# Performance work log

Hardware: AMD Instinct MI355X
Metric: run time of the kernel (lower is better)

Reference implementation:

```python
import jax, jax.numpy as jnp
import numpy as np

# fp4 e2m1 positive value grid and midpoints between adjacent grid values
_GRID = jnp.array([0.0, 0.5, 1.0, 1.5, 2.0, 3.0, 4.0, 6.0], dtype=jnp.float32)
_MIDS = jnp.array([0.25, 0.75, 1.25, 1.75, 2.5, 3.5, 5.0], dtype=jnp.float32)
BLOCK = 32               # MX block size
E8M0_BIAS = 127
F32_MIN_NORMAL = float(2.0 ** -126)
F4_E2M1_MAX_POW2 = 2     # log2 of largest power-of-two <= 6.0 -> 4.0


def _quantize_fp4(a):
    """Round-to-nearest-even onto the signed e2m1 grid."""
    mag = jnp.clip(jnp.abs(a), 0.0, 6.0)
    idx = jnp.searchsorted(_MIDS, mag, side='left')  # ties round down
    mids_pad = jnp.concatenate([_MIDS, jnp.array([-1.0], jnp.float32)])
    tie = mag == mids_pad[idx]
    idx = jnp.where(tie & (idx % 2 == 1), idx + 1, idx)  # ties-to-even mantissa
    return _GRID[idx] * jnp.where(a < 0, -1.0, 1.0)


def _floor_log2(m):
    """Exact floor(log2(m)) for m > 0, with corrections for fp rounding of log2."""
    e = jnp.floor(jnp.log2(m))
    e = jnp.where(jnp.exp2(e) > m, e - 1.0, e)
    e = jnp.where(jnp.exp2(e + 1.0) <= m, e + 1.0, e)
    return e


def _qdq_mxfp4(x):
    """Quantize-dequantize x to MX fp4_e2m1, block 32, FLOOR scale mode (to_mx + to_dtype)."""
    shp = x.shape
    xb = x.reshape(-1, BLOCK)
    max_abs = jnp.max(jnp.abs(xb), axis=1)
    eps = F32_MIN_NORMAL * (max_abs == 0).astype(jnp.float32)
    pow2 = _floor_log2(max_abs + eps)
    e_unb = jnp.clip(pow2 - F4_E2M1_MAX_POW2, -float(E8M0_BIAS), float(E8M0_BIAS) + 1.0)
    scale = jnp.maximum(jnp.exp2(e_unb), F32_MIN_NORMAL)  # [nblk]
    q = _quantize_fp4(xb / scale[:, None])
    return (q * scale[:, None]).reshape(shp)


def _dequant_weight(weight_packed, weight_scale, out_f, in_f):
    """Unpack uint8-packed fp4 (low nibble first), apply e8m0 block scales."""
    p = weight_packed.astype(jnp.int32)
    low = p & 0xF
    high = (p >> 4) & 0xF
    nib = jnp.stack([low, high], axis=-1).reshape(out_f, in_f)  # interleave low,high
    vals = _GRID[nib & 7] * jnp.where((nib & 8) > 0, -1.0, 1.0)
    s = jnp.exp2(weight_scale.astype(jnp.float32) - E8M0_BIAS)  # get_fp_scale(e8m0)
    return (vals.reshape(-1, BLOCK) * s[:, None]).reshape(out_f, in_f)


def setup_inputs() -> dict:
    key = jax.random.key(0)
    k1, k2, k3 = jax.random.split(key, 3)
    M, IN, OUT = 4096, 4096, 4096
    x = jax.random.normal(k1, (M, IN), dtype=jnp.float32)
    weight_packed = jax.random.randint(k2, (OUT, IN // 2), 0, 256, dtype=jnp.int32)
    weight_scale = jax.random.randint(k3, (OUT * IN // BLOCK,), 0, 135, dtype=jnp.int32)
    return {"x": x, "weight_packed": weight_packed, "weight_scale": weight_scale}


def reference(x, weight_packed, weight_scale):
    out_f = weight_packed.shape[0]
    in_f = weight_packed.shape[1] * 2
    xq = _qdq_mxfp4(x)                                       # qdq_mxfp4(x)
    w_dq = _dequant_weight(weight_packed, weight_scale, out_f, in_f)
    return xq @ w_dq.T                                       # matmul(x, w_dq.t())
```

## Files before the change

### kernel.cpp

```cpp
#include <hip/hip_runtime.h>
#include <stdint.h>

typedef __attribute__((ext_vector_type(4)))  int   intx4;
typedef __attribute__((ext_vector_type(8)))  int   intx8;
typedef __attribute__((ext_vector_type(16))) float floatx16;

#define GLL16(gp, lp)                                                               \
    __builtin_amdgcn_global_load_lds((const __attribute__((address_space(1))) unsigned int*)(gp), \
                                     (__attribute__((address_space(3))) unsigned int*)(lp), 16, 0, 0)
#define GLL4(gp, lp)                                                                \
    __builtin_amdgcn_global_load_lds((const __attribute__((address_space(1))) unsigned int*)(gp), \
                                     (__attribute__((address_space(3))) unsigned int*)(lp), 4, 0, 0)

__device__ __forceinline__ uint32_t enc1(float xv, float inv) {
    float a = fminf(fabsf(xv) * inv, 6.0f);
    int e;
    if (a < 2.0f)      e = (int)rintf(a + a);
    else if (a < 4.0f) e = (int)rintf(a) + 2;
    else               e = (int)rintf(a * 0.5f) + 4;
    return (uint32_t)e | ((__float_as_uint(xv) >> 28) & 8u);
}

__global__ __launch_bounds__(256) void prep_kernel(const float* __restrict__ x,
                                                   uint32_t* __restrict__ xq,
                                                   uint8_t* __restrict__ xs_t,
                                                   int nq, int M,
                                                   const int* __restrict__ wp,
                                                   uint32_t* __restrict__ wrep,
                                                   int nwb,
                                                   const int* __restrict__ wsc,
                                                   uint8_t* __restrict__ ws_t,
                                                   int N, int Ck) {
    const int bid = blockIdx.x;
    const int t = threadIdx.x;
    if (bid < nq) {
        const int gl = bid * 256 + t;
        const float4 v = ((const float4*)x)[gl];
        float m = fmaxf(fmaxf(fabsf(v.x), fabsf(v.y)), fmaxf(fabsf(v.z), fabsf(v.w)));
        m = fmaxf(m, __shfl_xor(m, 1));
        m = fmaxf(m, __shfl_xor(m, 2));
        m = fmaxf(m, __shfl_xor(m, 4));
        const unsigned ef = __float_as_uint(m) >> 23;
        const unsigned code = (ef < 3u) ? 1u : (ef - 2u);
        const float inv = __uint_as_float((254u - code) << 23);
        const uint32_t p = enc1(v.x, inv)        | (enc1(v.y, inv) << 4)
                         | (enc1(v.z, inv) << 8) | (enc1(v.w, inv) << 12);
        ((uint16_t*)xq)[gl] = (uint16_t)p;
        if ((gl & 7) == 0) {
            const int blk = gl >> 3;
            xs_t[(size_t)(blk & 127) * M + (blk >> 7)] = (uint8_t)code;
        }
        return;
    }
    if (bid < nq + nwb) {
        const int i = (bid - nq) * 256 + t;
        const int4 p = ((const int4*)wp)[i];
        wrep[i] = (uint32_t)(p.x & 0xFF) | ((uint32_t)(p.y & 0xFF) << 8)
                | ((uint32_t)(p.z & 0xFF) << 16) | ((uint32_t)(p.w & 0xFF) << 24);
        return;
    }
    __shared__ uint8_t raw[128 * 32];
    const int tidx = bid - nq - nwb;
    const int n0 = (tidx & 31) * 128;
    const int c0 = (tidx >> 5) * 32;
    {
        const int r = t >> 1, hf = t & 1;
        const size_t base = (size_t)(n0 + r) * Ck + c0 + hf * 16;
        uint32_t b[4];
#pragma unroll
        for (int j = 0; j < 4; ++j) {
            const int4 p = *(const int4*)(wsc + base + 4 * j);
            b[j] = (uint32_t)(p.x & 0xFF) | ((uint32_t)(p.y & 0xFF) << 8)
                 | ((uint32_t)(p.z & 0xFF) << 16) | ((uint32_t)(p.w & 0xFF) << 24);
        }
        *(uint4*)(raw + r * 32 + hf * 16) = make_uint4(b[0], b[1], b[2], b[3]);
    }
    __syncthreads();
    const int c = t >> 3, q = t & 7;
    uint32_t d[4];
#pragma unroll
    for (int j = 0; j < 4; ++j) {
        const int mb = q * 16 + j * 4;
        d[j] = (uint32_t)raw[(mb + 0) * 32 + c]
             | ((uint32_t)raw[(mb + 1) * 32 + c] << 8)
             | ((uint32_t)raw[(mb + 2) * 32 + c] << 16)
             | ((uint32_t)raw[(mb + 3) * 32 + c] << 24);
    }
    *(uint4*)(ws_t + (size_t)(c0 + c) * N + n0 + q * 16) = make_uint4(d[0], d[1], d[2], d[3]);
}

__global__ __launch_bounds__(256) void gemm_mx_kernel(const uint8_t* __restrict__ Apk,
                                                      const uint8_t* __restrict__ Bpk,
                                                      const uint8_t* __restrict__ AsT,
                                                      const uint8_t* __restrict__ BsT,
                                                      float* __restrict__ C,
                                                      int M, int N, int K) {
    __shared__ __align__(16) uint8_t sA[16384];
    __shared__ __align__(16) uint8_t sB[16384];
    __shared__ __align__(16) uint8_t sS[2048];

    const int tid = threadIdx.x;
    const int bm0 = blockIdx.y << 7;
    const int bn0 = blockIdx.x << 7;
    const int wave = tid >> 6;
    const int lane = tid & 63;
    const int wm = (wave >> 1) << 6;
    const int wn = (wave & 1) << 6;
    const int row = lane & 31;
    const int h = lane >> 5;
    const int Kb = K >> 1;

    const uint8_t* Ag[4];
    const uint8_t* Bg[4];
#pragma unroll
    for (int i = 0; i < 4; ++i) {
        const int s = tid + 256 * i;
        const int r = s >> 3;
        const int p = (s & 7) ^ (r & 7);
        Ag[i] = Apk + (size_t)(bm0 + r) * Kb + p * 16;
        Bg[i] = Bpk + (size_t)(bn0 + r) * Kb + p * 16;
    }

    const int st = tid & 127;
    const int sj = st >> 5, si = st & 31;
    const size_t sR = (size_t)((tid < 128) ? M : N);
    const uint8_t* Sg1 = ((tid < 128) ? (AsT + (size_t)sj * M + bm0)
                                      : (BsT + (size_t)sj * N + bn0)) + si * 4;
    const uint8_t* Sg2 = Sg1 + 4 * sR;
    const size_t sAdv = 8 * sR;
    const int soff = ((tid < 128) ? 0 : 1024) + st * 4;

    floatx16 acc[2][2];
#pragma unroll
    for (int a = 0; a < 2; ++a)
#pragma unroll
        for (int b = 0; b < 2; ++b)
#pragma unroll
            for (int r = 0; r < 16; ++r) acc[a][b][r] = 0.f;

    const int nchunk = K >> 8;
    const int ar0 = wm + row, ar1 = wm + 32 + row;
    const int br0 = wn + row, br1 = wn + 32 + row;

    for (int c = 0; c < nchunk; ++c) {
        __syncthreads();
        const size_t koff = (size_t)c << 7;
#pragma unroll
        for (int i = 0; i < 4; ++i) GLL16(Ag[i] + koff, sA + (tid + 256 * i) * 16);
#pragma unroll
        for (int i = 0; i < 4; ++i) GLL16(Bg[i] + koff, sB + (tid + 256 * i) * 16);
        GLL4(Sg1 + (size_t)c * sAdv, sS + soff);
        GLL4(Sg2 + (size_t)c * sAdv, sS + soff + 512);
        __syncthreads();

#pragma unroll
        for (int s = 0; s < 4; ++s) {
            const int kp = 2 * s + h;
            intx4 a4[2], b4[2];
            int sa[2], sb[2];
            a4[0] = *(const intx4*)(sA + ar0 * 128 + ((kp ^ (ar0 & 7)) << 4));
            a4[1] = *(const intx4*)(sA + ar1 * 128 + ((kp ^ (ar1 & 7)) << 4));
            b4[0] = *(const intx4*)(sB + br0 * 128 + ((kp ^ (br0 & 7)) << 4));
            b4[1] = *(const intx4*)(sB + br1 * 128 + ((kp ^ (br1 & 7)) << 4));
            sa[0] = sS[kp * 128 + ar0];
            sa[1] = sS[kp * 128 + ar1];
            sb[0] = sS[1024 + kp * 128 + br0];
            sb[1] = sS[1024 + kp * 128 + br1];
#pragma unroll
            for (int mt = 0; mt < 2; ++mt)
#pragma unroll
                for (int nt = 0; nt < 2; ++nt) {
                    intx8 a8 = {a4[mt][0], a4[mt][1], a4[mt][2], a4[mt][3], 0, 0, 0, 0};
                    intx8 b8 = {b4[nt][0], b4[nt][1], b4[nt][2], b4[nt][3], 0, 0, 0, 0};
                    acc[mt][nt] = __builtin_amdgcn_mfma_scale_f32_32x32x64_f8f6f4(
                        a8, b8, acc[mt][nt], 4, 4, 0, sa[mt], 0, sb[nt]);
                }
        }
    }

#pragma unroll
    for (int mt = 0; mt < 2; ++mt)
#pragma unroll
        for (int nt = 0; nt < 2; ++nt) {
            const int col = bn0 + wn + nt * 32 + row;
#pragma unroll
            for (int g = 0; g < 4; ++g) {
                const int rw = bm0 + wm + mt * 32 + 8 * g + 4 * h;
#pragma unroll
                for (int q = 0; q < 4; ++q)
                    C[(size_t)(rw + q) * N + col] = acc[mt][nt][4 * g + q];
            }
        }
}

extern "C" void kernel_launch(void* const* d_in, const int* in_sizes, int n_in,
                              void* d_out, int out_size, void* d_ws, size_t ws_size,
                              hipStream_t stream) {
    const float* x = (const float*)d_in[0];
    const int* wp = (const int*)d_in[1];
    const int* wsc = (const int*)d_in[2];
    float* out = (float*)d_out;

    const int K = 4096;
    const int M = in_sizes[0] / K;
    const int N = (in_sizes[1] * 2) / K;
    const int kbpr = K / 32;
    const int npack = N * K / 2;

    uint32_t* xq   = (uint32_t*)d_ws;
    uint8_t*  xs_t = (uint8_t*)d_ws + (size_t)M * K / 2;
    uint32_t* wrep = (uint32_t*)(xs_t + (size_t)M * kbpr);
    uint8_t*  ws_t = (uint8_t*)(wrep + (size_t)npack / 4);

    const int nq  = (M * K / 4) / 256;
    const int nwb = npack / 4 / 256;
    const int ntb = (N / 128) * (kbpr / 32);

    prep_kernel<<<nq + nwb + ntb, 256, 0, stream>>>(x, xq, xs_t, nq, M,
                                                    wp, wrep, nwb,
                                                    wsc, ws_t, N, kbpr);

    dim3 grid(N / 128, M / 128);
    gemm_mx_kernel<<<grid, 256, 0, stream>>>((const uint8_t*)xq, (const uint8_t*)wrep,
                                             xs_t, ws_t, out, M, N, K);
}
```

Before: 183.0 us.

## Interleave MX block scales by 8 k-blocks per row for vectorized loads

Changes the layout of the activation and weight e8m0 scale buffers from k-block-major transposed to groups of 8 consecutive k-block scales per row. The GEMM now reads each row's 8 scales for a K chunk with one 8-byte LDS load per tile and extracts them by shifting, replacing per-substep byte LDS reads. The prep kernel's scale transpose and activation scale writes are rewritten to match. Both global scale loads per chunk now read contiguous memory, at the cost of a few extra ALU shifts and selects.

```diff
diff --git a/kernel.cpp b/kernel.cpp
--- a/kernel.cpp
+++ b/kernel.cpp
@@ -23,13 +23,13 @@
 
 __global__ __launch_bounds__(256) void prep_kernel(const float* __restrict__ x,
                                                    uint32_t* __restrict__ xq,
-                                                   uint8_t* __restrict__ xs_t,
+                                                   uint8_t* __restrict__ xs_il,
                                                    int nq, int M,
                                                    const int* __restrict__ wp,
                                                    uint32_t* __restrict__ wrep,
                                                    int nwb,
                                                    const int* __restrict__ wsc,
-                                                   uint8_t* __restrict__ ws_t,
+                                                   uint8_t* __restrict__ ws_il,
                                                    int N, int Ck) {
     const int bid = blockIdx.x;
     const int t = threadIdx.x;
@@ -48,7 +48,9 @@
         ((uint16_t*)xq)[gl] = (uint16_t)p;
         if ((gl & 7) == 0) {
             const int blk = gl >> 3;
-            xs_t[(size_t)(blk & 127) * M + (blk >> 7)] = (uint8_t)code;
+            const int mm = blk >> 7, kb = blk & 127;
+            xs_il[(size_t)(kb >> 3) * ((size_t)M * 8) + (size_t)mm * 8 + (kb & 7)]
+                = (uint8_t)code;
         }
         return;
     }
@@ -76,23 +78,24 @@
         *(uint4*)(raw + r * 32 + hf * 16) = make_uint4(b[0], b[1], b[2], b[3]);
     }
     __syncthreads();
-    const int c = t >> 3, q = t & 7;
-    uint32_t d[4];
-#pragma unroll
-    for (int j = 0; j < 4; ++j) {
-        const int mb = q * 16 + j * 4;
-        d[j] = (uint32_t)raw[(mb + 0) * 32 + c]
-             | ((uint32_t)raw[(mb + 1) * 32 + c] << 8)
-             | ((uint32_t)raw[(mb + 2) * 32 + c] << 16)
-             | ((uint32_t)raw[(mb + 3) * 32 + c] << 24);
-    }
-    *(uint4*)(ws_t + (size_t)(c0 + c) * N + n0 + q * 16) = make_uint4(d[0], d[1], d[2], d[3]);
+    const int ml = t & 127;
+#pragma unroll
+    for (int pp = 0; pp < 2; ++pp) {
+        const int ckl = (t >> 7) * 2 + pp;
+        const int base = ml * 32 + ckl * 8;
+        const uint32_t lo = (uint32_t)raw[base + 0] | ((uint32_t)raw[base + 1] << 8)
+                          | ((uint32_t)raw[base + 2] << 16) | ((uint32_t)raw[base + 3] << 24);
+        const uint32_t hi = (uint32_t)raw[base + 4] | ((uint32_t)raw[base + 5] << 8)
+                          | ((uint32_t)raw[base + 6] << 16) | ((uint32_t)raw[base + 7] << 24);
+        *(uint2*)(ws_il + (size_t)(c0 / 8 + ckl) * ((size_t)N * 8)
+                        + (size_t)(n0 + ml) * 8) = make_uint2(lo, hi);
+    }
 }
 
 __global__ __launch_bounds__(256) void gemm_mx_kernel(const uint8_t* __restrict__ Apk,
                                                       const uint8_t* __restrict__ Bpk,
-                                                      const uint8_t* __restrict__ AsT,
-                                                      const uint8_t* __restrict__ BsT,
+                                                      const uint8_t* __restrict__ Asil,
+                                                      const uint8_t* __restrict__ Bsil,
                                                       float* __restrict__ C,
                                                       int M, int N, int K) {
     __shared__ __align__(16) uint8_t sA[16384];
@@ -122,12 +125,11 @@
     }
 
     const int st = tid & 127;
-    const int sj = st >> 5, si = st & 31;
-    const size_t sR = (size_t)((tid < 128) ? M : N);
-    const uint8_t* Sg1 = ((tid < 128) ? (AsT + (size_t)sj * M + bm0)
-                                      : (BsT + (size_t)sj * N + bn0)) + si * 4;
-    const uint8_t* Sg2 = Sg1 + 4 * sR;
-    const size_t sAdv = 8 * sR;
+    const size_t sRb = (size_t)((tid < 128) ? M : N) * 8;
+    const uint8_t* Sg1 = ((tid < 128) ? Asil + (size_t)(bm0 + (st >> 1)) * 8
+                                      : Bsil + (size_t)(bn0 + (st >> 1)) * 8)
+                         + (st & 1) * 4;
+    const uint8_t* Sg2 = Sg1 + 512;
     const int soff = ((tid < 128) ? 0 : 1024) + st * 4;
 
     floatx16 acc[2][2];
@@ -141,6 +143,8 @@
     const int nchunk = K >> 8;
     const int ar0 = wm + row, ar1 = wm + 32 + row;
     const int br0 = wn + row, br1 = wn + 32 + row;
+    const int shE = h * 8;
+    const int shO = 16 + h * 8;
 
     for (int c = 0; c < nchunk; ++c) {
         __syncthreads();
@@ -149,23 +153,30 @@
         for (int i = 0; i < 4; ++i) GLL16(Ag[i] + koff, sA + (tid + 256 * i) * 16);
 #pragma unroll
         for (int i = 0; i < 4; ++i) GLL16(Bg[i] + koff, sB + (tid + 256 * i) * 16);
-        GLL4(Sg1 + (size_t)c * sAdv, sS + soff);
-        GLL4(Sg2 + (size_t)c * sAdv, sS + soff + 512);
+        GLL4(Sg1 + (size_t)c * sRb, sS + soff);
+        GLL4(Sg2 + (size_t)c * sRb, sS + soff + 512);
         __syncthreads();
+
+        const uint2 sa0 = *(const uint2*)(sS + ar0 * 8);
+        const uint2 sa1 = *(const uint2*)(sS + ar1 * 8);
+        const uint2 sb0 = *(const uint2*)(sS + 1024 + br0 * 8);
+        const uint2 sb1 = *(const uint2*)(sS + 1024 + br1 * 8);
 
 #pragma unroll
         for (int s = 0; s < 4; ++s) {
             const int kp = 2 * s + h;
             intx4 a4[2], b4[2];
-            int sa[2], sb[2];
             a4[0] = *(const intx4*)(sA + ar0 * 128 + ((kp ^ (ar0 & 7)) << 4));
             a4[1] = *(const intx4*)(sA + ar1 * 128 + ((kp ^ (ar1 & 7)) << 4));
             b4[0] = *(const intx4*)(sB + br0 * 128 + ((kp ^ (br0 & 7)) << 4));
             b4[1] = *(const intx4*)(sB + br1 * 128 + ((kp ^ (br1 & 7)) << 4));
-            sa[0] = sS[kp * 128 + ar0];
-            sa[1] = sS[kp * 128 + ar1];
-            sb[0] = sS[1024 + kp * 128 + br0];
-            sb[1] = sS[1024 + kp * 128 + br1];
+            const uint32_t wa0 = (s & 2) ? sa0.y : sa0.x;
+            const uint32_t wa1 = (s & 2) ? sa1.y : sa1.x;
+            const uint32_t wb0 = (s & 2) ? sb0.y : sb0.x;
+            const uint32_t wb1 = (s & 2) ? sb1.y : sb1.x;
+            const int sh = (s & 1) ? shO : shE;
+            const int sa[2] = { (int)((wa0 >> sh) & 0xFF), (int)((wa1 >> sh) & 0xFF) };
+            const int sb[2] = { (int)((wb0 >> sh) & 0xFF), (int)((wb1 >> sh) & 0xFF) };
 #pragma unroll
             for (int mt = 0; mt < 2; ++mt)
 #pragma unroll
@@ -207,20 +218,20 @@
     const int kbpr = K / 32;
     const int npack = N * K / 2;
 
-    uint32_t* xq   = (uint32_t*)d_ws;
-    uint8_t*  xs_t = (uint8_t*)d_ws + (size_t)M * K / 2;
-    uint32_t* wrep = (uint32_t*)(xs_t + (size_t)M * kbpr);
-    uint8_t*  ws_t = (uint8_t*)(wrep + (size_t)npack / 4);
+    uint32_t* xq    = (uint32_t*)d_ws;
+    uint8_t*  xs_il = (uint8_t*)d_ws + (size_t)M * K / 2;
+    uint32_t* wrep  = (uint32_t*)(xs_il + (size_t)M * kbpr);
+    uint8_t*  ws_il = (uint8_t*)(wrep + (size_t)npack / 4);
 
     const int nq  = (M * K / 4) / 256;
     const int nwb = npack / 4 / 256;
     const int ntb = (N / 128) * (kbpr / 32);
 
-    prep_kernel<<<nq + nwb + ntb, 256, 0, stream>>>(x, xq, xs_t, nq, M,
+    prep_kernel<<<nq + nwb + ntb, 256, 0, stream>>>(x, xq, xs_il, nq, M,
                                                     wp, wrep, nwb,
-                                                    wsc, ws_t, N, kbpr);
+                                                    wsc, ws_il, N, kbpr);
 
     dim3 grid(N / 128, M / 128);
     gemm_mx_kernel<<<grid, 256, 0, stream>>>((const uint8_t*)xq, (const uint8_t*)wrep,
-                                             xs_t, ws_t, out, M, N, K);
-}
+                                             xs_il, ws_il, out, M, N, K);
+}
```

New measurement: 183.9 us. No clear change (+0.5%).
